# Optimization experiments

Measured on AMD Instinct MI355X. Metric: run time of the kernel, lower is better.

The kernel has to match this reference:

```python
import jax, jax.numpy as jnp
import numpy as np

B, T, C, H = 2, 2048, 1024, 16
HD = C // H  # 64


def setup_inputs() -> dict:
    key = jax.random.key(0)
    ks = jax.random.split(key, 5)
    x = jax.random.normal(ks[0], (B, T, C), jnp.float32)
    scale = 0.02
    Wq = jax.random.normal(ks[1], (C, C), jnp.float32) * scale
    Wk = jax.random.normal(ks[2], (C, C), jnp.float32) * scale
    Wv = jax.random.normal(ks[3], (C, C), jnp.float32) * scale
    Wo = jax.random.normal(ks[4], (C, C), jnp.float32) * scale
    # RoPE tables: freqs_cis = exp(i * pos * theta_j), theta_j = 10000^(-2j/HD)
    pos = jnp.arange(T, dtype=jnp.float32)
    theta = 10000.0 ** (-jnp.arange(0, HD, 2, dtype=jnp.float32) / HD)  # [HD/2]
    ang = pos[:, None] * theta[None, :]  # [T, HD/2]
    cos = jnp.cos(ang)
    sin = jnp.sin(ang)
    return {"x": x, "Wq": Wq, "Wk": Wk, "Wv": Wv, "Wo": Wo, "cos": cos, "sin": sin}


def _rope(t, cos, sin):
    # t: [B,T,H,HD]; pairs (even, odd) along last dim form complex numbers
    b, s, h, hd = t.shape
    tr = t.reshape(b, s, h, hd // 2, 2)
    t0, t1 = tr[..., 0], tr[..., 1]
    c = cos[None, :, None, :]  # [1,T,1,HD/2]
    sn = sin[None, :, None, :]
    o0 = t0 * c - t1 * sn
    o1 = t0 * sn + t1 * c
    return jnp.stack([o0, o1], axis=-1).reshape(b, s, h, hd)


def reference(x, Wq, Wk, Wv, Wo, cos, sin):
    b, t, c = x.shape
    h, hd = H, c // H
    q = (x @ Wq.T).reshape(b, t, h, hd)
    k = (x @ Wk.T).reshape(b, t, h, hd)
    v = (x @ Wv.T).reshape(b, t, h, hd)
    q = _rope(q, cos, sin)
    k = _rope(k, cos, sin)
    # explicit causal attention with full TxT score matrix (as in source)
    att = jnp.einsum("bthd,bshd->bhts", q, k) / jnp.sqrt(jnp.float32(hd))
    causal = jnp.tril(jnp.ones((t, t), dtype=bool))
    att = jnp.where(causal[None, None, :, :], att, -jnp.inf)
    att = jax.nn.softmax(att, axis=-1)
    out = jnp.einsum("bhts,bshd->bthd", att, v).reshape(b, t, c)
    return out @ Wo.T
```

## Files before the change

kernel.cpp:

```cpp
#include <hip/hip_runtime.h>
#include <cstdint>
#include <cstddef>


typedef __bf16 bf16;
typedef float  f32x4  __attribute__((ext_vector_type(4)));
typedef float  f32x16 __attribute__((ext_vector_type(16)));
typedef __bf16 bf16x4 __attribute__((ext_vector_type(4)));
typedef __bf16 bf16x8 __attribute__((ext_vector_type(8)));

constexpr int Bb = 2, Tt = 2048, Cc = 1024, Hh = 16;
constexpr int Mrows = Bb * Tt;
constexpr int NT = Tt / 64;
constexpr int LDS_ = 72;

#define GLOAD_LDS16(gp, lp)                                                      \
    __builtin_amdgcn_global_load_lds(                                            \
        (const __attribute__((address_space(1))) void*)(gp),                     \
        (__attribute__((address_space(3))) void*)(lp), 16, 0, 0)

#define QUAD_T(v0, v1, v2, v3, c2)                                               \
    {                                                                            \
        float e0 = (c2 & 1) ? v0 : v1, e1 = (c2 & 1) ? v2 : v3;                  \
        e0 = __shfl_xor(e0, 1); e1 = __shfl_xor(e1, 1);                          \
        if (c2 & 1) { v0 = e0; v2 = e1; } else { v1 = e0; v3 = e1; }             \
        float f0 = (c2 & 2) ? v0 : v2, f1 = (c2 & 2) ? v1 : v3;                  \
        f0 = __shfl_xor(f0, 2); f1 = __shfl_xor(f1, 2);                          \
        if (c2 & 2) { v0 = f0; v1 = f1; } else { v2 = f0; v3 = f1; }             \
    }

__device__ inline unsigned pkb(float a, float b)
{
    unsigned r;
    asm("v_cvt_pk_bf16_f32 %0, %1, %2" : "=v"(r) : "v"(a), "v"(b));
    return r;
}

__global__ __launch_bounds__(256) void convert_k(const float* __restrict__ x,
                                                 const float* __restrict__ Wq,
                                                 const float* __restrict__ Wk,
                                                 const float* __restrict__ Wv,
                                                 const float* __restrict__ Wo,
                                                 const float* __restrict__ cosb,
                                                 const float* __restrict__ sinb,
                                                 bf16* __restrict__ xb,
                                                 bf16* __restrict__ Wqkv,
                                                 bf16* __restrict__ Wob,
                                                 float2* __restrict__ cs)
{
    if (blockIdx.x >= 4096) {
        int pi = ((blockIdx.x - 4096) * 256 + threadIdx.x) * 8;
#pragma unroll
        for (int u = 0; u < 8; ++u)
            cs[pi + u] = float2{cosb[pi + u], sinb[pi + u]};
        return;
    }
    uint32_t id = blockIdx.x * 256 + threadIdx.x;
    const float* src; bf16* dst; float sc = 1.0f;
    if (id < 524288u) {
        uint32_t tile = id >> 10, slot = id & 1023;
        uint32_t row = (tile >> 4) * 128 + (slot >> 9) * 64 +
                       ((slot >> 6) & 3) * 16 + (slot & 15);
        uint32_t k = (tile & 15) * 64 + ((slot >> 8) & 1) * 32 + ((slot >> 4) & 3) * 8;
        src = x + (size_t)row * 1024 + k;
        dst = xb + (size_t)id * 8;
    } else if (id < 917504u) {
        uint32_t t2 = id - 524288u;
        uint32_t tile = t2 >> 10, slot = t2 & 1023;
        uint32_t n = (tile >> 4) * 128 + (slot >> 9) * 64 +
                     ((slot >> 6) & 3) * 16 + (slot & 15);
        uint32_t k = (tile & 15) * 64 + ((slot >> 8) & 1) * 32 + ((slot >> 4) & 3) * 8;
        if (n < 1024)      { src = Wq + (size_t)n * 1024 + k;
                             sc = 0.125f * 1.44269504088896f; }
        else if (n < 2048)   src = Wk + (size_t)(n - 1024) * 1024 + k;
        else                 src = Wv + (size_t)(n - 2048) * 1024 + k;
        dst = Wqkv + (size_t)t2 * 8;
    } else {
        uint32_t t3 = id - 917504u;
        uint32_t tile = t3 >> 9, slot = t3 & 511;
        uint32_t n = (tile >> 4) * 64 + (slot >> 8) * 32 +
                     ((slot >> 6) & 1) * 16 + (slot & 15);
        uint32_t k = (tile & 15) * 64 + ((slot >> 7) & 1) * 32 + ((slot >> 4) & 3) * 8;
        src = Wo + (size_t)n * 1024 + k;
        dst = Wob + (size_t)t3 * 8;
    }
    float4 v0 = *(const float4*)(src);
    float4 v1 = *(const float4*)(src + 4);
    bf16x8 t;
    t[0] = (bf16)(v0.x*sc); t[1] = (bf16)(v0.y*sc); t[2] = (bf16)(v0.z*sc); t[3] = (bf16)(v0.w*sc);
    t[4] = (bf16)(v1.x*sc); t[5] = (bf16)(v1.y*sc); t[6] = (bf16)(v1.z*sc); t[7] = (bf16)(v1.w*sc);
    *(bf16x8*)dst = t;
}

__global__ __launch_bounds__(256) void gemm_qkv(const bf16* __restrict__ A,
                                                const bf16* __restrict__ W,
                                                bf16* __restrict__ QK,
                                                bf16* __restrict__ Vt,
                                                const float2* __restrict__ cs)
{
    __shared__ bf16 As[8192];
    __shared__ bf16 Ws[8192];
    const int tid  = threadIdx.x;
    const int lane = tid & 63, wave = tid >> 6;
    const int rhw = wave >> 1, chw = wave & 1;
    const int wr = rhw * 64, wc = chw * 64;
    const int l16 = lane & 15, lq = lane >> 4;
    const int row0 = blockIdx.x * 128, col0 = blockIdx.y * 128;

    f32x4 acc[4][4];
#pragma unroll
    for (int i = 0; i < 4; ++i)
#pragma unroll
        for (int j = 0; j < 4; ++j) acc[i][j] = f32x4{0.f, 0.f, 0.f, 0.f};

    const bf16* At = A + (size_t)blockIdx.x * 16 * 8192;
    const bf16* Wt = W + (size_t)blockIdx.y * 16 * 8192;

    for (int kb = 0; kb < 16; ++kb) {
        const bf16* at = At + kb * 8192;
        const bf16* wt = Wt + kb * 8192;
#pragma unroll
        for (int rnd = 0; rnd < 4; ++rnd) {
            const int seg = rnd * 4 + wave;
            GLOAD_LDS16(at + seg * 512 + lane * 8, &As[seg * 512]);
            GLOAD_LDS16(wt + seg * 512 + lane * 8, &Ws[seg * 512]);
        }
        __syncthreads();
#pragma unroll
        for (int ks = 0; ks < 2; ++ks) {
            bf16x8 af[4], bfr[4];
#pragma unroll
            for (int i = 0; i < 4; ++i)
                af[i] = *(const bf16x8*)(&As[(rhw * 512 + ks * 256 + i * 64 + lq * 16 + l16) * 8]);
#pragma unroll
            for (int j = 0; j < 4; ++j)
                bfr[j] = *(const bf16x8*)(&Ws[(chw * 512 + ks * 256 + j * 64 + lq * 16 + l16) * 8]);
#pragma unroll
            for (int i = 0; i < 4; ++i)
#pragma unroll
                for (int j = 0; j < 4; ++j)
                    acc[i][j] = __builtin_amdgcn_mfma_f32_16x16x32_bf16(
                        af[i], bfr[j], acc[i][j], 0, 0, 0);
        }
        __syncthreads();
    }

    const int c2 = l16 & 3, g4 = (l16 >> 2) * 4;
    if (blockIdx.y < 16) {
#pragma unroll
        for (int i = 0; i < 4; ++i)
#pragma unroll
            for (int j = 0; j < 4; ++j) {
                float v0 = acc[i][j][0], v1 = acc[i][j][1];
                float v2 = acc[i][j][2], v3 = acc[i][j][3];
                QUAD_T(v0, v1, v2, v3, c2);
                const int row = row0 + wr + i * 16 + lq * 4 + c2;
                const int t   = row & (Tt - 1);
                const int colb = wc + j * 16 + g4;
                const int p0   = (colb & 63) >> 1;
                float4 cp = *(const float4*)(&cs[t * 32 + p0]);
                bf16x4 pk;
                pk[0] = (bf16)(v0 * cp.x - v1 * cp.y);
                pk[1] = (bf16)(v0 * cp.y + v1 * cp.x);
                pk[2] = (bf16)(v2 * cp.z - v3 * cp.w);
                pk[3] = (bf16)(v2 * cp.w + v3 * cp.z);
                *(bf16x4*)(&QK[(size_t)row * 2048 + col0 + colb]) = pk;
            }
    } else {
#pragma unroll
        for (int i = 0; i < 4; ++i)
#pragma unroll
            for (int j = 0; j < 4; ++j) {
                const int dfull = col0 - 2048 + wc + j * 16 + l16;
                const int h = dfull >> 6, d = dfull & 63;
                const int row = row0 + wr + i * 16 + lq * 4;
                const int b = row >> 11, t = row & (Tt - 1);
                bf16x4 pk;
                pk[0] = (bf16)acc[i][j][0]; pk[1] = (bf16)acc[i][j][1];
                pk[2] = (bf16)acc[i][j][2]; pk[3] = (bf16)acc[i][j][3];
                *(bf16x4*)(&Vt[((size_t)(b * 16 + h) * 64 + d) * (size_t)Tt + t]) = pk;
            }
    }
}

__global__ __launch_bounds__(256) void gemm_o(const bf16* __restrict__ A,
                                              const bf16* __restrict__ W,
                                              float* __restrict__ Out)
{
    __shared__ bf16 As[8192];
    __shared__ bf16 Ws[4096];
    const int tid  = threadIdx.x;
    const int lane = tid & 63, wave = tid >> 6;
    const int rhw = wave >> 1, chw = wave & 1;
    const int wr = rhw * 64, wc = chw * 32;
    const int l16 = lane & 15, lq = lane >> 4;
    const int row0 = blockIdx.x * 128, col0 = blockIdx.y * 64;

    f32x4 acc[4][2];
#pragma unroll
    for (int i = 0; i < 4; ++i)
#pragma unroll
        for (int j = 0; j < 2; ++j) acc[i][j] = f32x4{0.f, 0.f, 0.f, 0.f};

    const bf16* At = A + (size_t)blockIdx.x * 16 * 8192;
    const bf16* Wt = W + (size_t)blockIdx.y * 16 * 4096;

    for (int kb = 0; kb < 16; ++kb) {
        const bf16* at = At + kb * 8192;
        const bf16* wt = Wt + kb * 4096;
#pragma unroll
        for (int rnd = 0; rnd < 4; ++rnd) {
            const int seg = rnd * 4 + wave;
            GLOAD_LDS16(at + seg * 512 + lane * 8, &As[seg * 512]);
        }
#pragma unroll
        for (int rnd = 0; rnd < 2; ++rnd) {
            const int seg = rnd * 4 + wave;
            GLOAD_LDS16(wt + seg * 512 + lane * 8, &Ws[seg * 512]);
        }
        __syncthreads();
#pragma unroll
        for (int ks = 0; ks < 2; ++ks) {
            bf16x8 af[4], bfr[2];
#pragma unroll
            for (int i = 0; i < 4; ++i)
                af[i] = *(const bf16x8*)(&As[(rhw * 512 + ks * 256 + i * 64 + lq * 16 + l16) * 8]);
#pragma unroll
            for (int j = 0; j < 2; ++j)
                bfr[j] = *(const bf16x8*)(&Ws[(chw * 256 + ks * 128 + j * 64 + lq * 16 + l16) * 8]);
#pragma unroll
            for (int i = 0; i < 4; ++i)
#pragma unroll
                for (int j = 0; j < 2; ++j)
                    acc[i][j] = __builtin_amdgcn_mfma_f32_16x16x32_bf16(
                        af[i], bfr[j], acc[i][j], 0, 0, 0);
        }
        __syncthreads();
    }
    const int c2 = l16 & 3, g4 = (l16 >> 2) * 4;
#pragma unroll
    for (int i = 0; i < 4; ++i)
#pragma unroll
        for (int j = 0; j < 2; ++j) {
            float v0 = acc[i][j][0], v1 = acc[i][j][1];
            float v2 = acc[i][j][2], v3 = acc[i][j][3];
            QUAD_T(v0, v1, v2, v3, c2);
            const int row = row0 + wr + i * 16 + lq * 4 + c2;
            const int col = col0 + wc + j * 16 + g4;
            *(float4*)(&Out[(size_t)row * Cc + col]) = float4{v0, v1, v2, v3};
        }
}

__global__ __launch_bounds__(256, 2) void attn_k(const bf16* __restrict__ QK,
                                                 const bf16* __restrict__ Vt,
                                                 bf16* __restrict__ O)
{
    __shared__ bf16 Ks[2][64 * LDS_];
    __shared__ bf16 Vs[2][64 * LDS_];
    const int tid = threadIdx.x;
    const int wv = tid >> 6, lane = tid & 63;
    const int l31 = lane & 31, hf = lane >> 5;
    const int id = blockIdx.y * gridDim.x + blockIdx.x;
    const int bh = (id & 7) * 4 + ((id >> 3) & 3);
    const int sIdx = (id >> 5) & 7, rnd = id >> 8;
    const int gq = rnd ? (15 - sIdx) : sIdx;
    const int b = bh >> 4, h = bh & 15;
    const int nsteps = 2 * gq + 2;
    const int kr = tid >> 2, c0 = (tid & 3) * 16;

    const bf16* kcol = QK + 1024 + (size_t)(b * Tt + kr) * 2048 + h * 64 + c0;
    const bf16* vcol = Vt + ((size_t)bh * 64 + kr) * Tt + c0;

    const int qglob = gq * 128 + wv * 32 + l31;
    const bf16* qp = QK + (size_t)(b * Tt + qglob) * 2048 + h * 64 + hf * 8;
    bf16x8 qf[4];
#pragma unroll
    for (int kc = 0; kc < 4; ++kc)
        qf[kc] = *(const bf16x8*)(qp + kc * 16);

    uint4 pk0 = *(const uint4*)(kcol);
    uint4 pk1 = *(const uint4*)(kcol + 8);
    uint4 pv0 = *(const uint4*)(vcol);
    uint4 pv1 = *(const uint4*)(vcol + 8);
    *(uint4*)(&Ks[0][kr * LDS_ + c0])     = pk0;
    *(uint4*)(&Ks[0][kr * LDS_ + c0 + 8]) = pk1;
    *(uint4*)(&Vs[0][kr * LDS_ + c0])     = pv0;
    *(uint4*)(&Vs[0][kr * LDS_ + c0 + 8]) = pv1;
    __syncthreads();

    float la = 0.f, lb = 0.f, lc = 0.f, ld = 0.f;
    f32x16 o0, o1;
#pragma unroll
    for (int r = 0; r < 16; ++r) { o0[r] = 0.f; o1[r] = 0.f; }

    for (int t = 0; t < nsteps; ++t) {
        const int cur = t & 1;
        if (t + 1 < nsteps) {
            const bf16* kn = kcol + (size_t)(t + 1) * 64 * 2048;
            const bf16* vn = vcol + (t + 1) * 64;
            pk0 = *(const uint4*)(kn);
            pk1 = *(const uint4*)(kn + 8);
            pv0 = *(const uint4*)(vn);
            pv1 = *(const uint4*)(vn + 8);
        }

        f32x16 s0, s1;
#pragma unroll
        for (int r = 0; r < 16; ++r) { s0[r] = 0.f; s1[r] = 0.f; }
#pragma unroll
        for (int kc = 0; kc < 4; ++kc) {
            bf16x8 a = *(const bf16x8*)(&Ks[cur][l31 * LDS_ + kc * 16 + hf * 8]);
            s0 = __builtin_amdgcn_mfma_f32_32x32x16_bf16(a, qf[kc], s0, 0, 0, 0);
        }
#pragma unroll
        for (int kc = 0; kc < 4; ++kc) {
            bf16x8 a = *(const bf16x8*)(&Ks[cur][(32 + l31) * LDS_ + kc * 16 + hf * 8]);
            s1 = __builtin_amdgcn_mfma_f32_32x32x16_bf16(a, qf[kc], s1, 0, 0, 0);
        }
        if (t >= 2 * gq) {
            const int kbase = t * 64 + 4 * hf;
#pragma unroll
            for (int r = 0; r < 16; ++r) {
                const int key0 = kbase + (r & 3) + 8 * (r >> 2);
                if (key0 > qglob)      s0[r] = -1e30f;
                if (key0 + 32 > qglob) s1[r] = -1e30f;
            }
        }
#pragma unroll
        for (int r = 0; r < 16; ++r) {
            s0[r] = exp2f(s0[r]);
            s1[r] = exp2f(s1[r]);
            if (r & 1) { lb += s0[r]; ld += s1[r]; }
            else       { la += s0[r]; lc += s1[r]; }
        }
        bf16x8 pb[4];
#pragma unroll
        for (int c = 0; c < 4; ++c) {
            const f32x16& sv = (c < 2) ? s0 : s1;
            const int rb = (c & 1) * 8;
            unsigned X = pkb(sv[rb + 0], sv[rb + 1]);
            unsigned Y = pkb(sv[rb + 2], sv[rb + 3]);
            unsigned Z = pkb(sv[rb + 4], sv[rb + 5]);
            unsigned W = pkb(sv[rb + 6], sv[rb + 7]);
            asm("v_permlane32_swap_b32 %0, %1" : "+v"(X), "+v"(Z));
            asm("v_permlane32_swap_b32 %0, %1" : "+v"(Y), "+v"(W));
            union { unsigned u[4]; bf16x8 h; } tmp;
            tmp.u[0] = X; tmp.u[1] = Y; tmp.u[2] = Z; tmp.u[3] = W;
            pb[c] = tmp.h;
        }
#pragma unroll
        for (int c = 0; c < 4; ++c) {
            bf16x8 v = *(const bf16x8*)(&Vs[cur][l31 * LDS_ + c * 16 + hf * 8]);
            o0 = __builtin_amdgcn_mfma_f32_32x32x16_bf16(v, pb[c], o0, 0, 0, 0);
        }
#pragma unroll
        for (int c = 0; c < 4; ++c) {
            bf16x8 v = *(const bf16x8*)(&Vs[cur][(32 + l31) * LDS_ + c * 16 + hf * 8]);
            o1 = __builtin_amdgcn_mfma_f32_32x32x16_bf16(v, pb[c], o1, 0, 0, 0);
        }
        if (t + 1 < nsteps) {
            *(uint4*)(&Ks[cur ^ 1][kr * LDS_ + c0])     = pk0;
            *(uint4*)(&Ks[cur ^ 1][kr * LDS_ + c0 + 8]) = pk1;
            *(uint4*)(&Vs[cur ^ 1][kr * LDS_ + c0])     = pv0;
            *(uint4*)(&Vs[cur ^ 1][kr * LDS_ + c0 + 8]) = pv1;
        }
        __syncthreads();
    }
    float lsum = (la + lb) + (lc + ld);
    lsum += __shfl_xor(lsum, 32);
    float inv = 1.f / lsum;

    bf16* obase = O + ((size_t)(16 * b + gq) * 16 + h) * 8192;
    const int slot_row = (lane & 15) | (((2 * wv + ((lane >> 4) & 1)) & 3) << 6) |
                         (((wv >> 1) & 1) << 9);
#pragma unroll
    for (int dt = 0; dt < 2; ++dt) {
        const f32x16& ov = dt ? o1 : o0;
#pragma unroll
        for (int g = 0; g < 4; ++g) {
            bf16x4 pk;
#pragma unroll
            for (int r = 0; r < 4; ++r) pk[r] = (bf16)(ov[4 * g + r] * inv);
            const int slot = slot_row | (g << 4) | (dt << 8);
            *(bf16x4*)(obase + slot * 8 + 4 * hf) = pk;
        }
    }
}

extern "C" void kernel_launch(void* const* d_in, const int* in_sizes, int n_in,
                              void* d_out, int out_size, void* d_ws, size_t ws_size,
                              hipStream_t stream)
{
    const float* x    = (const float*)d_in[0];
    const float* Wq   = (const float*)d_in[1];
    const float* Wk   = (const float*)d_in[2];
    const float* Wv   = (const float*)d_in[3];
    const float* Wo   = (const float*)d_in[4];
    const float* cosb = (const float*)d_in[5];
    const float* sinb = (const float*)d_in[6];

    constexpr size_t M1 = 1024 * 1024;
    bf16* base = (bf16*)d_ws;
    bf16*   xb   = base;
    bf16*   QK   = base + 4 * M1;
    bf16*   VtG  = base + 12 * M1;
    bf16*   Wqkv = base + 16 * M1;
    bf16*   Wob  = base + 19 * M1;
    float2* csT  = (float2*)(base + 20 * M1);
    bf16*   Ow   = xb;

    convert_k<<<4096 + 32, 256, 0, stream>>>(x, Wq, Wk, Wv, Wo, cosb, sinb,
                                             xb, Wqkv, Wob, csT);

    gemm_qkv<<<dim3(Mrows / 128, 3072 / 128), 256, 0, stream>>>(
        xb, Wqkv, QK, VtG, csT);

    attn_k<<<dim3(32, 16), 256, 0, stream>>>(QK, VtG, Ow);

    gemm_o<<<dim3(Mrows / 128, Cc / 64), 256, 0, stream>>>(Ow, Wob, (float*)d_out);
}
```

Measured before the change: 183.3 us.

## Shrink attention blocks to 64 query rows and compute row sums via MFMA

The attention kernel now uses 128-thread blocks that each handle a 64-row query tile, which doubles the grid. Longest-first ordering across four rounds balances the causal workload at the finer granularity. The scalar per-lane exp-sum accumulation and cross-half shuffle are replaced by an extra MFMA against a ones vector, so the denominator comes out of the matrix unit. Each block now does only one masked diagonal step instead of two. In exchange, each block loads K/V tiles for fewer queries, so K/V reuse per load falls and global traffic rises, and the extra MFMAs add matrix-unit work.

Measured after the change: 223.7 us. 1.22x slower.

```diff
diff --git a/kernel.cpp b/kernel.cpp
--- a/kernel.cpp
+++ b/kernel.cpp
@@ -251,7 +251,7 @@
         }
 }
 
-__global__ __launch_bounds__(256, 2) void attn_k(const bf16* __restrict__ QK,
+__global__ __launch_bounds__(128, 2) void attn_k(const bf16* __restrict__ QK,
                                                  const bf16* __restrict__ Vt,
                                                  bf16* __restrict__ O)
 {
@@ -262,46 +262,53 @@
     const int l31 = lane & 31, hf = lane >> 5;
     const int id = blockIdx.y * gridDim.x + blockIdx.x;
     const int bh = (id & 7) * 4 + ((id >> 3) & 3);
-    const int sIdx = (id >> 5) & 7, rnd = id >> 8;
-    const int gq = rnd ? (15 - sIdx) : sIdx;
+    const int s8 = (id >> 5) & 7, rnd4 = id >> 8;
+    const int qt = (rnd4 == 0) ? 31 - s8 : (rnd4 == 1) ? 16 + s8
+                 : (rnd4 == 2) ? 15 - s8 : s8;
     const int b = bh >> 4, h = bh & 15;
-    const int nsteps = 2 * gq + 2;
-    const int kr = tid >> 2, c0 = (tid & 3) * 16;
+    const int kr = tid >> 1, c0 = (tid & 1) * 32;
 
     const bf16* kcol = QK + 1024 + (size_t)(b * Tt + kr) * 2048 + h * 64 + c0;
     const bf16* vcol = Vt + ((size_t)bh * 64 + kr) * Tt + c0;
 
-    const int qglob = gq * 128 + wv * 32 + l31;
+    const int qglob = qt * 64 + wv * 32 + l31;
     const bf16* qp = QK + (size_t)(b * Tt + qglob) * 2048 + h * 64 + hf * 8;
     bf16x8 qf[4];
 #pragma unroll
     for (int kc = 0; kc < 4; ++kc)
         qf[kc] = *(const bf16x8*)(qp + kc * 16);
 
-    uint4 pk0 = *(const uint4*)(kcol);
-    uint4 pk1 = *(const uint4*)(kcol + 8);
-    uint4 pv0 = *(const uint4*)(vcol);
-    uint4 pv1 = *(const uint4*)(vcol + 8);
-    *(uint4*)(&Ks[0][kr * LDS_ + c0])     = pk0;
-    *(uint4*)(&Ks[0][kr * LDS_ + c0 + 8]) = pk1;
-    *(uint4*)(&Vs[0][kr * LDS_ + c0])     = pv0;
-    *(uint4*)(&Vs[0][kr * LDS_ + c0 + 8]) = pv1;
+    bf16x8 onef;
+#pragma unroll
+    for (int r = 0; r < 8; ++r) onef[r] = (bf16)1.0f;
+
+    uint4 pk[4], pv[4];
+#pragma unroll
+    for (int u = 0; u < 4; ++u) {
+        pk[u] = *(const uint4*)(kcol + u * 8);
+        pv[u] = *(const uint4*)(vcol + u * 8);
+    }
+#pragma unroll
+    for (int u = 0; u < 4; ++u) {
+        *(uint4*)(&Ks[0][kr * LDS_ + c0 + u * 8]) = pk[u];
+        *(uint4*)(&Vs[0][kr * LDS_ + c0 + u * 8]) = pv[u];
+    }
     __syncthreads();
 
-    float la = 0.f, lb = 0.f, lc = 0.f, ld = 0.f;
-    f32x16 o0, o1;
-#pragma unroll
-    for (int r = 0; r < 16; ++r) { o0[r] = 0.f; o1[r] = 0.f; }
-
-    for (int t = 0; t < nsteps; ++t) {
+    f32x16 o0, o1, accl;
+#pragma unroll
+    for (int r = 0; r < 16; ++r) { o0[r] = 0.f; o1[r] = 0.f; accl[r] = 0.f; }
+
+    for (int t = 0; t <= qt; ++t) {
         const int cur = t & 1;
-        if (t + 1 < nsteps) {
+        if (t < qt) {
             const bf16* kn = kcol + (size_t)(t + 1) * 64 * 2048;
             const bf16* vn = vcol + (t + 1) * 64;
-            pk0 = *(const uint4*)(kn);
-            pk1 = *(const uint4*)(kn + 8);
-            pv0 = *(const uint4*)(vn);
-            pv1 = *(const uint4*)(vn + 8);
+#pragma unroll
+            for (int u = 0; u < 4; ++u) {
+                pk[u] = *(const uint4*)(kn + u * 8);
+                pv[u] = *(const uint4*)(vn + u * 8);
+            }
         }
 
         f32x16 s0, s1;
@@ -317,7 +324,7 @@
             bf16x8 a = *(const bf16x8*)(&Ks[cur][(32 + l31) * LDS_ + kc * 16 + hf * 8]);
             s1 = __builtin_amdgcn_mfma_f32_32x32x16_bf16(a, qf[kc], s1, 0, 0, 0);
         }
-        if (t >= 2 * gq) {
+        if (t == qt) {
             const int kbase = t * 64 + 4 * hf;
 #pragma unroll
             for (int r = 0; r < 16; ++r) {
@@ -330,8 +337,6 @@
         for (int r = 0; r < 16; ++r) {
             s0[r] = exp2f(s0[r]);
             s1[r] = exp2f(s1[r]);
-            if (r & 1) { lb += s0[r]; ld += s1[r]; }
-            else       { la += s0[r]; lc += s1[r]; }
         }
         bf16x8 pb[4];
 #pragma unroll
@@ -348,6 +353,10 @@
             tmp.u[0] = X; tmp.u[1] = Y; tmp.u[2] = Z; tmp.u[3] = W;
             pb[c] = tmp.h;
         }
+        accl = __builtin_amdgcn_mfma_f32_32x32x16_bf16(onef, pb[0], accl, 0, 0, 0);
+        accl = __builtin_amdgcn_mfma_f32_32x32x16_bf16(onef, pb[1], accl, 0, 0, 0);
+        accl = __builtin_amdgcn_mfma_f32_32x32x16_bf16(onef, pb[2], accl, 0, 0, 0);
+        accl = __builtin_amdgcn_mfma_f32_32x32x16_bf16(onef, pb[3], accl, 0, 0, 0);
 #pragma unroll
         for (int c = 0; c < 4; ++c) {
             bf16x8 v = *(const bf16x8*)(&Vs[cur][l31 * LDS_ + c * 16 + hf * 8]);
@@ -358,31 +367,31 @@
             bf16x8 v = *(const bf16x8*)(&Vs[cur][(32 + l31) * LDS_ + c * 16 + hf * 8]);
             o1 = __builtin_amdgcn_mfma_f32_32x32x16_bf16(v, pb[c], o1, 0, 0, 0);
         }
-        if (t + 1 < nsteps) {
-            *(uint4*)(&Ks[cur ^ 1][kr * LDS_ + c0])     = pk0;
-            *(uint4*)(&Ks[cur ^ 1][kr * LDS_ + c0 + 8]) = pk1;
-            *(uint4*)(&Vs[cur ^ 1][kr * LDS_ + c0])     = pv0;
-            *(uint4*)(&Vs[cur ^ 1][kr * LDS_ + c0 + 8]) = pv1;
+        if (t < qt) {
+#pragma unroll
+            for (int u = 0; u < 4; ++u) {
+                *(uint4*)(&Ks[cur ^ 1][kr * LDS_ + c0 + u * 8]) = pk[u];
+                *(uint4*)(&Vs[cur ^ 1][kr * LDS_ + c0 + u * 8]) = pv[u];
+            }
         }
         __syncthreads();
     }
-    float lsum = (la + lb) + (lc + ld);
-    lsum += __shfl_xor(lsum, 32);
-    float inv = 1.f / lsum;
-
-    bf16* obase = O + ((size_t)(16 * b + gq) * 16 + h) * 8192;
+    float inv = 1.f / accl[0];
+
+    bf16* obase = O + ((size_t)(16 * b + (qt >> 1)) * 16 + h) * 8192;
+    const int rh = qt & 1;
     const int slot_row = (lane & 15) | (((2 * wv + ((lane >> 4) & 1)) & 3) << 6) |
-                         (((wv >> 1) & 1) << 9);
+                         (rh << 9);
 #pragma unroll
     for (int dt = 0; dt < 2; ++dt) {
         const f32x16& ov = dt ? o1 : o0;
 #pragma unroll
         for (int g = 0; g < 4; ++g) {
-            bf16x4 pk;
-#pragma unroll
-            for (int r = 0; r < 4; ++r) pk[r] = (bf16)(ov[4 * g + r] * inv);
+            bf16x4 pk4;
+#pragma unroll
+            for (int r = 0; r < 4; ++r) pk4[r] = (bf16)(ov[4 * g + r] * inv);
             const int slot = slot_row | (g << 4) | (dt << 8);
-            *(bf16x4*)(obase + slot * 8 + 4 * hf) = pk;
+            *(bf16x4*)(obase + slot * 8 + 4 * hf) = pk4;
         }
     }
 }
@@ -415,7 +424,7 @@
     gemm_qkv<<<dim3(Mrows / 128, 3072 / 128), 256, 0, stream>>>(
         xb, Wqkv, QK, VtG, csT);
 
-    attn_k<<<dim3(32, 16), 256, 0, stream>>>(QK, VtG, Ow);
+    attn_k<<<dim3(32, 32), 128, 0, stream>>>(QK, VtG, Ow);
 
     gemm_o<<<dim3(Mrows / 128, Cc / 64), 256, 0, stream>>>(Ow, Wob, (float*)d_out);
 }
```
